# Performance work log

Hardware: AMD Instinct MI355X
Metric: run time of the kernel (lower is better)

Reference implementation:

```python
import jax, jax.numpy as jnp
import numpy as np

WS = 7
NH = 4

def _rel_idx(ws):
    ch, cw = np.meshgrid(np.arange(ws), np.arange(ws), indexing='ij')
    cf = np.stack([ch.ravel(), cw.ravel()])  # [2, ws*ws]
    rel = cf[:, :, None] - cf[:, None, :]
    rel = rel.transpose(1, 2, 0)
    rel[:, :, 0] += ws - 1
    rel[:, :, 1] += ws - 1
    rel[:, :, 0] *= 2 * ws - 1
    return jnp.asarray(rel.sum(-1), dtype=jnp.int32)  # [N, N]

def layernorm(x, g, b, eps=1e-5):
    m = jnp.mean(x, -1, keepdims=True)
    v = jnp.var(x, -1, keepdims=True)
    return (x - m) * jax.lax.rsqrt(v + eps) * g + b

def setup_inputs() -> dict:
    key = jax.random.key(0)
    ks = jax.random.split(key, 8)
    B, HH, WW, C = 32, 56, 56, 128
    hid = 512
    s = 0.02
    return {
        'x': jax.random.normal(ks[0], (B, HH * WW, C), jnp.float32),
        'H': HH, 'W': WW,
        'norm1_g': jnp.ones((C,), jnp.float32),
        'norm1_b': jnp.zeros((C,), jnp.float32),
        'qkv_w': jax.random.normal(ks[1], (3 * C, C), jnp.float32) * s,
        'qkv_b': jnp.zeros((3 * C,), jnp.float32),
        'rel_bias_table': jax.random.normal(ks[2], ((2 * WS - 1) ** 2, NH), jnp.float32) * s,
        'rel_idx': _rel_idx(WS),
        'proj_w': jax.random.normal(ks[3], (C, C), jnp.float32) * s,
        'proj_b': jnp.zeros((C,), jnp.float32),
        'norm2_g': jnp.ones((C,), jnp.float32),
        'norm2_b': jnp.zeros((C,), jnp.float32),
        'mlp_w1': jax.random.normal(ks[4], (hid, C), jnp.float32) * s,
        'mlp_b1': jnp.zeros((hid,), jnp.float32),
        'mlp_w2': jax.random.normal(ks[5], (C, hid), jnp.float32) * s,
        'mlp_b2': jnp.zeros((C,), jnp.float32),
    }

def swin_block(x, H, W, norm1_g, norm1_b, qkv_w, qkv_b, rel_bias_table, rel_idx,
               proj_w, proj_b, norm2_g, norm2_b, mlp_w1, mlp_b1, mlp_w2, mlp_b2,
               shift=3, ws=WS, nh=NH):
    B, L, C = x.shape
    N = ws * ws
    hd = C // nh
    scale = hd ** -0.5
    shortcut = x
    h = layernorm(x, norm1_g, norm1_b).reshape(B, H, W, C)
    if shift > 0:
        h = jnp.roll(h, (-shift, -shift), axis=(1, 2))
    # window partition -> [B*nW, N, C]
    h = h.reshape(B, H // ws, ws, W // ws, ws, C).transpose(0, 1, 3, 2, 4, 5).reshape(-1, N, C)
    # attention (no mask in source forward)
    qkv = h @ qkv_w.T + qkv_b  # [B_, N, 3C]
    qkv = qkv.reshape(-1, N, 3, nh, hd).transpose(2, 0, 3, 1, 4)
    q, k, v = qkv[0] * scale, qkv[1], qkv[2]  # [B_, nh, N, hd]
    attn = jnp.einsum('bhnd,bhmd->bhnm', q, k)
    bias = rel_bias_table[rel_idx.reshape(-1)].reshape(N, N, nh).transpose(2, 0, 1)
    attn = jax.nn.softmax(attn + bias[None], axis=-1)
    o = jnp.einsum('bhnm,bhmd->bhnd', attn, v).transpose(0, 2, 1, 3).reshape(-1, N, C)
    o = o @ proj_w.T + proj_b
    # window reverse -> [B, H, W, C]
    o = o.reshape(B, H // ws, W // ws, ws, ws, C).transpose(0, 1, 3, 2, 4, 5).reshape(B, H, W, C)
    if shift > 0:
        o = jnp.roll(o, (shift, shift), axis=(1, 2))
    x = shortcut + o.reshape(B, L, C)
    h2 = layernorm(x, norm2_g, norm2_b)
    h2 = jax.nn.gelu(h2 @ mlp_w1.T + mlp_b1, approximate=False) @ mlp_w2.T + mlp_b2
    return x + h2

def reference(x, H, W, norm1_g, norm1_b, qkv_w, qkv_b, rel_bias_table, rel_idx,
              proj_w, proj_b, norm2_g, norm2_b, mlp_w1, mlp_b1, mlp_w2, mlp_b2):
    return swin_block(x, H, W, norm1_g, norm1_b, qkv_w, qkv_b, rel_bias_table, rel_idx,
                      proj_w, proj_b, norm2_g, norm2_b, mlp_w1, mlp_b1, mlp_w2, mlp_b2)
```

## Files before the change

### kernel.cpp

```cpp
#include <hip/hip_runtime.h>
#include <hip/hip_bf16.h>


#define NWIN 2048

typedef short short8  __attribute__((ext_vector_type(8)));
typedef short short4v __attribute__((ext_vector_type(4)));
typedef float f32x4   __attribute__((ext_vector_type(4)));

#define QKVW_OFF  0
#define PROJW_OFF 49152
#define W1_OFF    65536
#define W2_OFF    131072
#define BIAS_BYTE_OFF 393216

__device__ __forceinline__ short f2bs(float v) {
  __hip_bfloat16 h = __float2bfloat16(v);
  union { __hip_bfloat16 h; short s; } u; u.h = h; return u.s;
}
__device__ __forceinline__ float gelu_f(float v) {
  float u = v * (0.7978845608028654f + 0.03567740814f * v * v);
  return v * __builtin_amdgcn_rcpf(1.f + __expf(-2.f * u));
}

__global__ __launch_bounds__(256) void conv_kernel(
    const float* __restrict__ qkvw, const float* __restrict__ projw,
    const float* __restrict__ w1,   const float* __restrict__ w2,
    const float* __restrict__ tab,  const int* __restrict__ ridx,
    __hip_bfloat16* __restrict__ wsb, float* __restrict__ biasT)
{
  int idx = blockIdx.x * 256 + threadIdx.x;
  if (idx < 49152)       wsb[QKVW_OFF + idx]          = __float2bfloat16(qkvw[idx]);
  else if (idx < 65536)  wsb[PROJW_OFF + idx - 49152] = __float2bfloat16(projw[idx - 49152]);
  else if (idx < 131072) wsb[W1_OFF + idx - 65536]    = __float2bfloat16(w1[idx - 65536]);
  else if (idx < 196608) wsb[W2_OFF + idx - 131072]   = __float2bfloat16(w2[idx - 131072]);
  else if (idx < 212992) {
    int i = idx - 196608;
    int h = i >> 12, m = (i >> 6) & 63, n = i & 63;
    biasT[i] = (m < 49 && n < 49) ? tab[ridx[n*49 + m]*4 + h] : 0.f;
  }
}

__global__ __launch_bounds__(512, 4) void fused_kernel(
    const float* __restrict__ x,
    const float* __restrict__ n1g, const float* __restrict__ n1b,
    const __hip_bfloat16* __restrict__ qkvwb, const float* __restrict__ qkvb,
    const float* __restrict__ biasT,
    const __hip_bfloat16* __restrict__ projwb, const float* __restrict__ projb,
    const float* __restrict__ n2g, const float* __restrict__ n2b,
    const __hip_bfloat16* __restrict__ w1b, const float* __restrict__ b1,
    const __hip_bfloat16* __restrict__ w2b, const float* __restrict__ b2,
    float* __restrict__ out)
{
  __shared__ alignas(16) __hip_bfloat16 hbuf[64][136];
  __shared__ alignas(16) char regA[40960];
  __shared__ alignas(16) __hip_bfloat16 vT[4][32][72];
  __hip_bfloat16* const qkb = (__hip_bfloat16*)regA;
  float*          const x2s = (float*)regA;
  __hip_bfloat16* const hb  = (__hip_bfloat16*)regA;

  const int tid = threadIdx.x, wave = tid >> 6, lane = tid & 63;
  const int l15 = lane & 15, quad = lane >> 4;
  const int b = blockIdx.x >> 6, wi = (blockIdx.x >> 3) & 7, wj = blockIdx.x & 7;

  {
    float g0 = n1g[lane], g1 = n1g[lane+64], e0 = n1b[lane], e1 = n1b[lane+64];
    for (int n = wave; n < 49; n += 8) {
      int r = n / 7, c = n - r * 7;
      int si = wi*7 + r + 3; if (si >= 56) si -= 56;
      int sj = wj*7 + c + 3; if (sj >= 56) sj -= 56;
      const float* xr = x + (b*3136 + si*56 + sj) * 128;
      float v0 = xr[lane], v1 = xr[lane + 64];
      float s = v0 + v1, sq = v0*v0 + v1*v1;
      #pragma unroll
      for (int off = 32; off > 0; off >>= 1) {
        s  += __shfl_xor(s,  off);
        sq += __shfl_xor(sq, off);
      }
      float mean = s * 0.0078125f;
      float var  = sq * 0.0078125f - mean*mean;
      float rstd = rsqrtf(var + 1e-5f);
      hbuf[n][lane]    = __float2bfloat16((v0-mean)*rstd*g0 + e0);
      hbuf[n][lane+64] = __float2bfloat16((v1-mean)*rstd*g1 + e1);
    }
  }
  __syncthreads();

  {
    const int t0 = wave * 3;
    f32x4 acc[3][4] = {};
    #pragma unroll
    for (int ks = 0; ks < 4; ++ks) {
      short8 hf[4];
      #pragma unroll
      for (int mt = 0; mt < 4; ++mt)
        hf[mt] = *(const short8*)(&hbuf[mt*16 + l15][ks*32 + quad*8]);
      #pragma unroll
      for (int ft = 0; ft < 3; ++ft) {
        short8 wf = *(const short8*)(qkvwb + ((t0 + ft)*16 + l15)*128 + ks*32 + quad*8);
        #pragma unroll
        for (int mt = 0; mt < 4; ++mt)
          acc[ft][mt] = __builtin_amdgcn_mfma_f32_16x16x32_bf16(wf, hf[mt], acc[ft][mt], 0, 0, 0);
      }
    }
    #pragma unroll
    for (int ft = 0; ft < 3; ++ft) {
      const int t = t0 + ft;
      if (t < 16) {
        const int which = t >> 3;
        const int fo = (t & 7) * 16 + quad * 4;
        const int hh = fo >> 5, d0 = fo & 31;
        const float qs = (t < 8) ? 0.17677669529663687f : 1.0f;
        float bb[4];
        #pragma unroll
        for (int r = 0; r < 4; ++r) bb[r] = qkvb[which*128 + fo + r];
        #pragma unroll
        for (int mt = 0; mt < 4; ++mt) {
          int m = mt*16 + l15;
          if (m < 49) {
            short4v pk;
            #pragma unroll
            for (int r = 0; r < 4; ++r) pk[r] = f2bs((acc[ft][mt][r] + bb[r]) * qs);
            *(short4v*)(qkb + ((hh*2 + which)*64 + m)*40 + d0) = pk;
          }
        }
      } else {
        const int nf = (t - 16) * 16 + quad * 4;
        const int hh = nf >> 5, d0 = nf & 31;
        float bb[4];
        #pragma unroll
        for (int r = 0; r < 4; ++r) bb[r] = qkvb[256 + nf + r];
        #pragma unroll
        for (int mt = 0; mt < 4; ++mt) {
          int m = mt*16 + l15;
          #pragma unroll
          for (int r = 0; r < 4; ++r) {
            float v = (m < 49) ? (acc[ft][mt][r] + bb[r]) : 0.f;
            vT[hh][d0 + r][m] = __float2bfloat16(v);
          }
        }
      }
    }
  }
  __syncthreads();

  {
    const int h = wave >> 1, half = wave & 1;
    __hip_bfloat16* qbase = qkb + (h*2 + 0)*64*40;
    __hip_bfloat16* kbase = qkb + (h*2 + 1)*64*40;
    short8 kf[4], qf[2];
    #pragma unroll
    for (int mt = 0; mt < 4; ++mt) kf[mt] = *(const short8*)(kbase + (mt*16 + l15)*40 + quad*8);
    #pragma unroll
    for (int nt = 0; nt < 2; ++nt)
      qf[nt] = *(const short8*)(qbase + ((half*2 + nt)*16 + l15)*40 + quad*8);
    __syncthreads();

    f32x4 sacc[4][2] = {};
    #pragma unroll
    for (int mt = 0; mt < 4; ++mt)
      #pragma unroll
      for (int nt = 0; nt < 2; ++nt)
        sacc[mt][nt] = __builtin_amdgcn_mfma_f32_16x16x32_bf16(kf[mt], qf[nt], sacc[mt][nt], 0, 0, 0);

    const float* bT = biasT + h*4096;
    #pragma unroll
    for (int mt = 0; mt < 4; ++mt)
      #pragma unroll
      for (int nt = 0; nt < 2; ++nt)
        #pragma unroll
        for (int r = 0; r < 4; ++r)
          sacc[mt][nt][r] += bT[(mt*16 + quad*4 + r)*64 + (half*2 + nt)*16 + l15];

    __hip_bfloat16* pb = qbase;
    #pragma unroll
    for (int nt = 0; nt < 2; ++nt) {
      float mx = -1e30f;
      #pragma unroll
      for (int mt = 0; mt < 3; ++mt)
        #pragma unroll
        for (int r = 0; r < 4; ++r) mx = fmaxf(mx, sacc[mt][nt][r]);
      mx = fmaxf(mx, (quad == 0) ? sacc[3][nt][0] : -1e30f);
      mx = fmaxf(mx, __shfl_xor(mx, 16));
      mx = fmaxf(mx, __shfl_xor(mx, 32));
      float sum = 0.f;
      #pragma unroll
      for (int mt = 0; mt < 3; ++mt)
        #pragma unroll
        for (int r = 0; r < 4; ++r) {
          float e = __expf(sacc[mt][nt][r] - mx);
          sacc[mt][nt][r] = e; sum += e;
        }
      {
        float e = (quad == 0) ? __expf(sacc[3][nt][0] - mx) : 0.f;
        sacc[3][nt][0] = e; sacc[3][nt][1] = 0.f; sacc[3][nt][2] = 0.f; sacc[3][nt][3] = 0.f;
        sum += e;
      }
      sum += __shfl_xor(sum, 16);
      sum += __shfl_xor(sum, 32);
      float inv = 1.f / sum;
      int n = (half*2 + nt)*16 + l15;
      #pragma unroll
      for (int mt = 0; mt < 4; ++mt) {
        short4v pk;
        #pragma unroll
        for (int r = 0; r < 4; ++r) pk[r] = f2bs(sacc[mt][nt][r] * inv);
        *(short4v*)(pb + n*72 + mt*16 + quad*4) = pk;
      }
    }

    f32x4 oacc[2][2] = {};
    #pragma unroll
    for (int kt = 0; kt < 2; ++kt) {
      short8 vf[2], pf[2];
      #pragma unroll
      for (int dt = 0; dt < 2; ++dt)
        vf[dt] = *(const short8*)(&vT[h][dt*16 + l15][kt*32 + quad*8]);
      #pragma unroll
      for (int nc = 0; nc < 2; ++nc)
        pf[nc] = *(const short8*)(pb + ((half*2 + nc)*16 + l15)*72 + kt*32 + quad*8);
      #pragma unroll
      for (int dt = 0; dt < 2; ++dt)
        #pragma unroll
        for (int nc = 0; nc < 2; ++nc)
          oacc[dt][nc] = __builtin_amdgcn_mfma_f32_16x16x32_bf16(vf[dt], pf[nc], oacc[dt][nc], 0, 0, 0);
    }
    #pragma unroll
    for (int dt = 0; dt < 2; ++dt)
      #pragma unroll
      for (int nc = 0; nc < 2; ++nc) {
        int n = (half*2 + nc)*16 + l15;
        if (n < 49) {
          short4v pk;
          #pragma unroll
          for (int r = 0; r < 4; ++r) pk[r] = f2bs(oacc[dt][nc][r]);
          *(short4v*)(&hbuf[n][h*32 + dt*16 + quad*4]) = pk;
        }
      }
  }
  __syncthreads();

  f32x4 x2v[4];
  {
    const int ncol0 = wave * 16;
    f32x4 acc[4] = {};
    #pragma unroll
    for (int ks = 0; ks < 4; ++ks) {
      short8 af[4];
      #pragma unroll
      for (int mt = 0; mt < 4; ++mt)
        af[mt] = *(const short8*)(&hbuf[mt*16 + l15][ks*32 + quad*8]);
      short8 bfr = *(const short8*)(projwb + (ncol0 + l15)*128 + ks*32 + quad*8);
      #pragma unroll
      for (int mt = 0; mt < 4; ++mt)
        acc[mt] = __builtin_amdgcn_mfma_f32_16x16x32_bf16(af[mt], bfr, acc[mt], 0, 0, 0);
    }
    int n = ncol0 + l15;
    float pbv = projb[n];
    #pragma unroll
    for (int mt = 0; mt < 4; ++mt) {
      #pragma unroll
      for (int r = 0; r < 4; ++r) {
        int m = mt*16 + quad*4 + r;
        float v = 0.f;
        if (m < 49) {
          int rr = m / 7, cc = m - rr * 7;
          int si = wi*7 + rr + 3; if (si >= 56) si -= 56;
          int sj = wj*7 + cc + 3; if (sj >= 56) sj -= 56;
          int o = (b*3136 + si*56 + sj) * 128 + n;
          v = acc[mt][r] + pbv + x[o];
        }
        x2v[mt][r] = v;
        x2s[m*132 + n] = v;
      }
    }
  }
  __syncthreads();

  {
    float g0 = n2g[lane], g1 = n2g[lane+64], e0 = n2b[lane], e1 = n2b[lane+64];
    for (int n = wave; n < 49; n += 8) {
      float v0 = x2s[n*132 + lane], v1 = x2s[n*132 + lane + 64];
      float s = v0 + v1, sq = v0*v0 + v1*v1;
      #pragma unroll
      for (int off = 32; off > 0; off >>= 1) {
        s  += __shfl_xor(s,  off);
        sq += __shfl_xor(sq, off);
      }
      float mean = s * 0.0078125f;
      float var  = sq * 0.0078125f - mean*mean;
      float rstd = rsqrtf(var + 1e-5f);
      hbuf[n][lane]    = __float2bfloat16((v0-mean)*rstd*g0 + e0);
      hbuf[n][lane+64] = __float2bfloat16((v1-mean)*rstd*g1 + e1);
    }
    __hip_bfloat16 z = __float2bfloat16(0.f);
    for (int n = 49 + wave; n < 64; n += 8) {
      hbuf[n][lane] = z; hbuf[n][lane+64] = z;
    }
  }
  __syncthreads();

  f32x4 acc2[4] = {};
  #pragma unroll
  for (int chunk = 0; chunk < 2; ++chunk) {
    {
      const int jbl = wave * 32;
      f32x4 acc1[2][4] = {};
      #pragma unroll
      for (int ks = 0; ks < 4; ++ks) {
        short8 lf[4];
        #pragma unroll
        for (int mt = 0; mt < 4; ++mt)
          lf[mt] = *(const short8*)(&hbuf[mt*16 + l15][ks*32 + quad*8]);
        #pragma unroll
        for (int jt = 0; jt < 2; ++jt) {
          short8 wf = *(const short8*)(w1b + (chunk*256 + jbl + jt*16 + l15)*128 + ks*32 + quad*8);
          #pragma unroll
          for (int mt = 0; mt < 4; ++mt)
            acc1[jt][mt] = __builtin_amdgcn_mfma_f32_16x16x32_bf16(wf, lf[mt], acc1[jt][mt], 0, 0, 0);
        }
      }
      #pragma unroll
      for (int jt = 0; jt < 2; ++jt) {
        int j0l = jbl + jt*16 + quad*4;
        float bb[4];
        #pragma unroll
        for (int r = 0; r < 4; ++r) bb[r] = b1[chunk*256 + j0l + r];
        #pragma unroll
        for (int mt = 0; mt < 4; ++mt) {
          int m = mt*16 + l15;
          short4v pk;
          #pragma unroll
          for (int r = 0; r < 4; ++r) pk[r] = f2bs(gelu_f(acc1[jt][mt][r] + bb[r]));
          *(short4v*)(hb + m*264 + j0l) = pk;
        }
      }
    }
    __syncthreads();

    {
      const int fb2 = wave * 16;
      #pragma unroll
      for (int ks = 0; ks < 8; ++ks) {
        short8 af[4];
        #pragma unroll
        for (int mt = 0; mt < 4; ++mt)
          af[mt] = *(const short8*)(hb + (mt*16 + l15)*264 + ks*32 + quad*8);
        short8 bfr = *(const short8*)(w2b + (fb2 + l15)*512 + chunk*256 + ks*32 + quad*8);
        #pragma unroll
        for (int mt = 0; mt < 4; ++mt)
          acc2[mt] = __builtin_amdgcn_mfma_f32_16x16x32_bf16(af[mt], bfr, acc2[mt], 0, 0, 0);
      }
    }
    if (chunk == 0) __syncthreads();
  }

  {
    const int f = wave * 16 + l15;
    const float bb = b2[f];
    #pragma unroll
    for (int mt = 0; mt < 4; ++mt) {
      #pragma unroll
      for (int r = 0; r < 4; ++r) {
        int m = mt*16 + quad*4 + r;
        if (m < 49) {
          int rr = m / 7, cc = m - rr * 7;
          int si = wi*7 + rr + 3; if (si >= 56) si -= 56;
          int sj = wj*7 + cc + 3; if (sj >= 56) sj -= 56;
          int o = (b*3136 + si*56 + sj) * 128 + f;
          out[o] = acc2[mt][r] + bb + x2v[mt][r];
        }
      }
    }
  }
}

extern "C" void kernel_launch(void* const* d_in, const int* in_sizes, int n_in,
                              void* d_out, int out_size, void* d_ws, size_t ws_size,
                              hipStream_t stream) {
  const float* x     = (const float*)d_in[0];
  const float* n1g   = (const float*)d_in[3];
  const float* n1b   = (const float*)d_in[4];
  const float* qkvw  = (const float*)d_in[5];
  const float* qkvb  = (const float*)d_in[6];
  const float* tab   = (const float*)d_in[7];
  const int*   ridx  = (const int*)d_in[8];
  const float* projw = (const float*)d_in[9];
  const float* projb = (const float*)d_in[10];
  const float* n2g   = (const float*)d_in[11];
  const float* n2b   = (const float*)d_in[12];
  const float* w1    = (const float*)d_in[13];
  const float* b1    = (const float*)d_in[14];
  const float* w2    = (const float*)d_in[15];
  const float* b2    = (const float*)d_in[16];
  float* outp = (float*)d_out;

  __hip_bfloat16* wsb = (__hip_bfloat16*)d_ws;
  float* biasT = (float*)((char*)d_ws + BIAS_BYTE_OFF);

  hipLaunchKernelGGL(conv_kernel, dim3(832), dim3(256), 0, stream,
                     qkvw, projw, w1, w2, tab, ridx, wsb, biasT);
  hipLaunchKernelGGL(fused_kernel, dim3(NWIN), dim3(512), 0, stream,
                     x, n1g, n1b, wsb + QKVW_OFF, qkvb, biasT, wsb + PROJW_OFF, projb,
                     n2g, n2b, wsb + W1_OFF, b1, wsb + W2_OFF, b2, outp);
}
```

Measured before the change: 268.8 us.

## Double threads per window block to 1024 and split work across 16 waves

Raises the fused window kernel from 8 to 16 waves per block and repartitions every stage: the QKV, proj and MLP2 GEMMs split rows into two 32-row halves, attention gives each wave one head and one 16-query tile, and MLP1 gives each wave 16 hidden columns. The aim is more latency hiding and more parallel waves per window, with fewer accumulators per wave. The cost is duplicated weight-fragment loads across the row halves, possible register-budget pressure from launch_bounds(1024,8), and shared memory that still caps how many blocks fit per CU.

```diff
diff --git a/kernel.cpp b/kernel.cpp
--- a/kernel.cpp
+++ b/kernel.cpp
@@ -41,7 +41,7 @@
   }
 }
 
-__global__ __launch_bounds__(512, 4) void fused_kernel(
+__global__ __launch_bounds__(1024, 8) void fused_kernel(
     const float* __restrict__ x,
     const float* __restrict__ n1g, const float* __restrict__ n1b,
     const __hip_bfloat16* __restrict__ qkvwb, const float* __restrict__ qkvb,
@@ -61,11 +61,12 @@
 
   const int tid = threadIdx.x, wave = tid >> 6, lane = tid & 63;
   const int l15 = lane & 15, quad = lane >> 4;
+  const int wlo = wave & 7, mh = wave >> 3;
   const int b = blockIdx.x >> 6, wi = (blockIdx.x >> 3) & 7, wj = blockIdx.x & 7;
 
   {
     float g0 = n1g[lane], g1 = n1g[lane+64], e0 = n1b[lane], e1 = n1b[lane+64];
-    for (int n = wave; n < 49; n += 8) {
+    for (int n = wave; n < 49; n += 16) {
       int r = n / 7, c = n - r * 7;
       int si = wi*7 + r + 3; if (si >= 56) si -= 56;
       int sj = wj*7 + c + 3; if (sj >= 56) sj -= 56;
@@ -87,19 +88,19 @@
   __syncthreads();
 
   {
-    const int t0 = wave * 3;
-    f32x4 acc[3][4] = {};
+    const int t0 = wlo * 3;
+    f32x4 acc[3][2] = {};
     #pragma unroll
     for (int ks = 0; ks < 4; ++ks) {
-      short8 hf[4];
-      #pragma unroll
-      for (int mt = 0; mt < 4; ++mt)
-        hf[mt] = *(const short8*)(&hbuf[mt*16 + l15][ks*32 + quad*8]);
+      short8 hf[2];
+      #pragma unroll
+      for (int mt = 0; mt < 2; ++mt)
+        hf[mt] = *(const short8*)(&hbuf[mh*32 + mt*16 + l15][ks*32 + quad*8]);
       #pragma unroll
       for (int ft = 0; ft < 3; ++ft) {
         short8 wf = *(const short8*)(qkvwb + ((t0 + ft)*16 + l15)*128 + ks*32 + quad*8);
         #pragma unroll
-        for (int mt = 0; mt < 4; ++mt)
+        for (int mt = 0; mt < 2; ++mt)
           acc[ft][mt] = __builtin_amdgcn_mfma_f32_16x16x32_bf16(wf, hf[mt], acc[ft][mt], 0, 0, 0);
       }
     }
@@ -115,8 +116,8 @@
         #pragma unroll
         for (int r = 0; r < 4; ++r) bb[r] = qkvb[which*128 + fo + r];
         #pragma unroll
-        for (int mt = 0; mt < 4; ++mt) {
-          int m = mt*16 + l15;
+        for (int mt = 0; mt < 2; ++mt) {
+          int m = mh*32 + mt*16 + l15;
           if (m < 49) {
             short4v pk;
             #pragma unroll
@@ -131,8 +132,8 @@
         #pragma unroll
         for (int r = 0; r < 4; ++r) bb[r] = qkvb[256 + nf + r];
         #pragma unroll
-        for (int mt = 0; mt < 4; ++mt) {
-          int m = mt*16 + l15;
+        for (int mt = 0; mt < 2; ++mt) {
+          int m = mh*32 + mt*16 + l15;
           #pragma unroll
           for (int r = 0; r < 4; ++r) {
             float v = (m < 49) ? (acc[ft][mt][r] + bb[r]) : 0.f;
@@ -145,42 +146,35 @@
   __syncthreads();
 
   {
-    const int h = wave >> 1, half = wave & 1;
+    const int h = wave >> 2, nt = wave & 3;
     __hip_bfloat16* qbase = qkb + (h*2 + 0)*64*40;
     __hip_bfloat16* kbase = qkb + (h*2 + 1)*64*40;
-    short8 kf[4], qf[2];
+    short8 kf[4], qf;
     #pragma unroll
     for (int mt = 0; mt < 4; ++mt) kf[mt] = *(const short8*)(kbase + (mt*16 + l15)*40 + quad*8);
-    #pragma unroll
-    for (int nt = 0; nt < 2; ++nt)
-      qf[nt] = *(const short8*)(qbase + ((half*2 + nt)*16 + l15)*40 + quad*8);
+    qf = *(const short8*)(qbase + (nt*16 + l15)*40 + quad*8);
     __syncthreads();
 
-    f32x4 sacc[4][2] = {};
+    f32x4 sacc[4] = {};
     #pragma unroll
     for (int mt = 0; mt < 4; ++mt)
-      #pragma unroll
-      for (int nt = 0; nt < 2; ++nt)
-        sacc[mt][nt] = __builtin_amdgcn_mfma_f32_16x16x32_bf16(kf[mt], qf[nt], sacc[mt][nt], 0, 0, 0);
+      sacc[mt] = __builtin_amdgcn_mfma_f32_16x16x32_bf16(kf[mt], qf, sacc[mt], 0, 0, 0);
 
     const float* bT = biasT + h*4096;
     #pragma unroll
     for (int mt = 0; mt < 4; ++mt)
       #pragma unroll
-      for (int nt = 0; nt < 2; ++nt)
-        #pragma unroll
-        for (int r = 0; r < 4; ++r)
-          sacc[mt][nt][r] += bT[(mt*16 + quad*4 + r)*64 + (half*2 + nt)*16 + l15];
+      for (int r = 0; r < 4; ++r)
+        sacc[mt][r] += bT[(mt*16 + quad*4 + r)*64 + nt*16 + l15];
 
     __hip_bfloat16* pb = qbase;
-    #pragma unroll
-    for (int nt = 0; nt < 2; ++nt) {
+    {
       float mx = -1e30f;
       #pragma unroll
       for (int mt = 0; mt < 3; ++mt)
         #pragma unroll
-        for (int r = 0; r < 4; ++r) mx = fmaxf(mx, sacc[mt][nt][r]);
-      mx = fmaxf(mx, (quad == 0) ? sacc[3][nt][0] : -1e30f);
+        for (int r = 0; r < 4; ++r) mx = fmaxf(mx, sacc[mt][r]);
+      mx = fmaxf(mx, (quad == 0) ? sacc[3][0] : -1e30f);
       mx = fmaxf(mx, __shfl_xor(mx, 16));
       mx = fmaxf(mx, __shfl_xor(mx, 32));
       float sum = 0.f;
@@ -188,80 +182,73 @@
       for (int mt = 0; mt < 3; ++mt)
         #pragma unroll
         for (int r = 0; r < 4; ++r) {
-          float e = __expf(sacc[mt][nt][r] - mx);
-          sacc[mt][nt][r] = e; sum += e;
+          float e = __expf(sacc[mt][r] - mx);
+          sacc[mt][r] = e; sum += e;
         }
       {
-        float e = (quad == 0) ? __expf(sacc[3][nt][0] - mx) : 0.f;
-        sacc[3][nt][0] = e; sacc[3][nt][1] = 0.f; sacc[3][nt][2] = 0.f; sacc[3][nt][3] = 0.f;
+        float e = (quad == 0) ? __expf(sacc[3][0] - mx) : 0.f;
+        sacc[3][0] = e; sacc[3][1] = 0.f; sacc[3][2] = 0.f; sacc[3][3] = 0.f;
         sum += e;
       }
       sum += __shfl_xor(sum, 16);
       sum += __shfl_xor(sum, 32);
       float inv = 1.f / sum;
-      int n = (half*2 + nt)*16 + l15;
+      int n = nt*16 + l15;
       #pragma unroll
       for (int mt = 0; mt < 4; ++mt) {
         short4v pk;
         #pragma unroll
-        for (int r = 0; r < 4; ++r) pk[r] = f2bs(sacc[mt][nt][r] * inv);
+        for (int r = 0; r < 4; ++r) pk[r] = f2bs(sacc[mt][r] * inv);
         *(short4v*)(pb + n*72 + mt*16 + quad*4) = pk;
       }
     }
 
-    f32x4 oacc[2][2] = {};
+    f32x4 oacc[2] = {};
     #pragma unroll
     for (int kt = 0; kt < 2; ++kt) {
-      short8 vf[2], pf[2];
+      short8 vf[2], pf;
       #pragma unroll
       for (int dt = 0; dt < 2; ++dt)
         vf[dt] = *(const short8*)(&vT[h][dt*16 + l15][kt*32 + quad*8]);
-      #pragma unroll
-      for (int nc = 0; nc < 2; ++nc)
-        pf[nc] = *(const short8*)(pb + ((half*2 + nc)*16 + l15)*72 + kt*32 + quad*8);
+      pf = *(const short8*)(pb + (nt*16 + l15)*72 + kt*32 + quad*8);
       #pragma unroll
       for (int dt = 0; dt < 2; ++dt)
-        #pragma unroll
-        for (int nc = 0; nc < 2; ++nc)
-          oacc[dt][nc] = __builtin_amdgcn_mfma_f32_16x16x32_bf16(vf[dt], pf[nc], oacc[dt][nc], 0, 0, 0);
-    }
-    #pragma unroll
-    for (int dt = 0; dt < 2; ++dt)
-      #pragma unroll
-      for (int nc = 0; nc < 2; ++nc) {
-        int n = (half*2 + nc)*16 + l15;
-        if (n < 49) {
-          short4v pk;
-          #pragma unroll
-          for (int r = 0; r < 4; ++r) pk[r] = f2bs(oacc[dt][nc][r]);
-          *(short4v*)(&hbuf[n][h*32 + dt*16 + quad*4]) = pk;
-        }
-      }
-  }
-  __syncthreads();
-
-  f32x4 x2v[4];
-  {
-    const int ncol0 = wave * 16;
-    f32x4 acc[4] = {};
+        oacc[dt] = __builtin_amdgcn_mfma_f32_16x16x32_bf16(vf[dt], pf, oacc[dt], 0, 0, 0);
+    }
+    #pragma unroll
+    for (int dt = 0; dt < 2; ++dt) {
+      int n = nt*16 + l15;
+      if (n < 49) {
+        short4v pk;
+        #pragma unroll
+        for (int r = 0; r < 4; ++r) pk[r] = f2bs(oacc[dt][r]);
+        *(short4v*)(&hbuf[n][h*32 + dt*16 + quad*4]) = pk;
+      }
+    }
+  }
+  __syncthreads();
+
+  f32x4 x2v[2];
+  {
+    f32x4 acc[2] = {};
     #pragma unroll
     for (int ks = 0; ks < 4; ++ks) {
-      short8 af[4];
-      #pragma unroll
-      for (int mt = 0; mt < 4; ++mt)
-        af[mt] = *(const short8*)(&hbuf[mt*16 + l15][ks*32 + quad*8]);
-      short8 bfr = *(const short8*)(projwb + (ncol0 + l15)*128 + ks*32 + quad*8);
-      #pragma unroll
-      for (int mt = 0; mt < 4; ++mt)
+      short8 af[2];
+      #pragma unroll
+      for (int mt = 0; mt < 2; ++mt)
+        af[mt] = *(const short8*)(&hbuf[mh*32 + mt*16 + l15][ks*32 + quad*8]);
+      short8 bfr = *(const short8*)(projwb + (wlo*16 + l15)*128 + ks*32 + quad*8);
+      #pragma unroll
+      for (int mt = 0; mt < 2; ++mt)
         acc[mt] = __builtin_amdgcn_mfma_f32_16x16x32_bf16(af[mt], bfr, acc[mt], 0, 0, 0);
     }
-    int n = ncol0 + l15;
+    int n = wlo*16 + l15;
     float pbv = projb[n];
     #pragma unroll
-    for (int mt = 0; mt < 4; ++mt) {
+    for (int mt = 0; mt < 2; ++mt) {
       #pragma unroll
       for (int r = 0; r < 4; ++r) {
-        int m = mt*16 + quad*4 + r;
+        int m = mh*32 + mt*16 + quad*4 + r;
         float v = 0.f;
         if (m < 49) {
           int rr = m / 7, cc = m - rr * 7;
@@ -279,7 +266,7 @@
 
   {
     float g0 = n2g[lane], g1 = n2g[lane+64], e0 = n2b[lane], e1 = n2b[lane+64];
-    for (int n = wave; n < 49; n += 8) {
+    for (int n = wave; n < 49; n += 16) {
       float v0 = x2s[n*132 + lane], v1 = x2s[n*132 + lane + 64];
       float s = v0 + v1, sq = v0*v0 + v1*v1;
       #pragma unroll
@@ -294,61 +281,54 @@
       hbuf[n][lane+64] = __float2bfloat16((v1-mean)*rstd*g1 + e1);
     }
     __hip_bfloat16 z = __float2bfloat16(0.f);
-    for (int n = 49 + wave; n < 64; n += 8) {
+    for (int n = 49 + wave; n < 64; n += 16) {
       hbuf[n][lane] = z; hbuf[n][lane+64] = z;
     }
   }
   __syncthreads();
 
-  f32x4 acc2[4] = {};
+  f32x4 acc2[2] = {};
   #pragma unroll
   for (int chunk = 0; chunk < 2; ++chunk) {
     {
-      const int jbl = wave * 32;
-      f32x4 acc1[2][4] = {};
+      const int jg = chunk*256 + wave*16;
+      f32x4 acc1[4] = {};
       #pragma unroll
       for (int ks = 0; ks < 4; ++ks) {
         short8 lf[4];
         #pragma unroll
         for (int mt = 0; mt < 4; ++mt)
           lf[mt] = *(const short8*)(&hbuf[mt*16 + l15][ks*32 + quad*8]);
-        #pragma unroll
-        for (int jt = 0; jt < 2; ++jt) {
-          short8 wf = *(const short8*)(w1b + (chunk*256 + jbl + jt*16 + l15)*128 + ks*32 + quad*8);
-          #pragma unroll
-          for (int mt = 0; mt < 4; ++mt)
-            acc1[jt][mt] = __builtin_amdgcn_mfma_f32_16x16x32_bf16(wf, lf[mt], acc1[jt][mt], 0, 0, 0);
-        }
-      }
-      #pragma unroll
-      for (int jt = 0; jt < 2; ++jt) {
-        int j0l = jbl + jt*16 + quad*4;
-        float bb[4];
-        #pragma unroll
-        for (int r = 0; r < 4; ++r) bb[r] = b1[chunk*256 + j0l + r];
-        #pragma unroll
-        for (int mt = 0; mt < 4; ++mt) {
-          int m = mt*16 + l15;
-          short4v pk;
-          #pragma unroll
-          for (int r = 0; r < 4; ++r) pk[r] = f2bs(gelu_f(acc1[jt][mt][r] + bb[r]));
-          *(short4v*)(hb + m*264 + j0l) = pk;
-        }
+        short8 wf = *(const short8*)(w1b + (jg + l15)*128 + ks*32 + quad*8);
+        #pragma unroll
+        for (int mt = 0; mt < 4; ++mt)
+          acc1[mt] = __builtin_amdgcn_mfma_f32_16x16x32_bf16(wf, lf[mt], acc1[mt], 0, 0, 0);
+      }
+      int j0l = wave*16 + quad*4;
+      float bb[4];
+      #pragma unroll
+      for (int r = 0; r < 4; ++r) bb[r] = b1[chunk*256 + j0l + r];
+      #pragma unroll
+      for (int mt = 0; mt < 4; ++mt) {
+        int m = mt*16 + l15;
+        short4v pk;
+        #pragma unroll
+        for (int r = 0; r < 4; ++r) pk[r] = f2bs(gelu_f(acc1[mt][r] + bb[r]));
+        *(short4v*)(hb + m*264 + j0l) = pk;
       }
     }
     __syncthreads();
 
     {
-      const int fb2 = wave * 16;
       #pragma unroll
       for (int ks = 0; ks < 8; ++ks) {
-        short8 af[4];
-        #pragma unroll
-        for (int mt = 0; mt < 4; ++mt)
-          af[mt] = *(const short8*)(hb + (mt*16 + l15)*264 + ks*32 + quad*8);
-        short8 bfr = *(const short8*)(w2b + (fb2 + l15)*512 + chunk*256 + ks*32 + quad*8);
-        #pragma unroll
-        for (int mt = 0; mt < 4; ++mt)
+        short8 af[2];
+        #pragma unroll
+        for (int mt = 0; mt < 2; ++mt)
+          af[mt] = *(const short8*)(hb + (mh*32 + mt*16 + l15)*264 + ks*32 + quad*8);
+        short8 bfr = *(const short8*)(w2b + (wlo*16 + l15)*512 + chunk*256 + ks*32 + quad*8);
+        #pragma unroll
+        for (int mt = 0; mt < 2; ++mt)
           acc2[mt] = __builtin_amdgcn_mfma_f32_16x16x32_bf16(af[mt], bfr, acc2[mt], 0, 0, 0);
       }
     }
@@ -356,13 +336,13 @@
   }
 
   {
-    const int f = wave * 16 + l15;
+    const int f = wlo*16 + l15;
     const float bb = b2[f];
     #pragma unroll
-    for (int mt = 0; mt < 4; ++mt) {
+    for (int mt = 0; mt < 2; ++mt) {
       #pragma unroll
       for (int r = 0; r < 4; ++r) {
-        int m = mt*16 + quad*4 + r;
+        int m = mh*32 + mt*16 + quad*4 + r;
         if (m < 49) {
           int rr = m / 7, cc = m - rr * 7;
           int si = wi*7 + rr + 3; if (si >= 56) si -= 56;
@@ -400,7 +380,7 @@
 
   hipLaunchKernelGGL(conv_kernel, dim3(832), dim3(256), 0, stream,
                      qkvw, projw, w1, w2, tab, ridx, wsb, biasT);
-  hipLaunchKernelGGL(fused_kernel, dim3(NWIN), dim3(512), 0, stream,
+  hipLaunchKernelGGL(fused_kernel, dim3(NWIN), dim3(1024), 0, stream,
                      x, n1g, n1b, wsb + QKVW_OFF, qkvb, biasT, wsb + PROJW_OFF, projb,
                      n2g, n2b, wsb + W1_OFF, b1, wsb + W2_OFF, b2, outp);
 }
```

New measurement: 345.5 us. 1.29x slower.
